# Optimization experiments

Measured on AMD Instinct MI355X. Metric: run time of the kernel, lower is better.

## Reference

```python
import jax, jax.numpy as jnp
import numpy as np

DIST_POWER = 1  # distance_power from init

def setup_inputs() -> dict:
    key = jax.random.key(0)
    k1, k2 = jax.random.split(key)
    N, D, C = 8192, 128, 256
    l_embeds = jax.random.normal(k1, (N, D), dtype=jnp.float32)
    l_labels = jax.random.randint(k2, (N,), 0, C, dtype=jnp.int64)
    return {"l_embeds": l_embeds, "l_labels": l_labels}

def reference(l_embeds, l_labels):
    # normalize_embeds=True
    x = l_embeds / jnp.linalg.norm(l_embeds, axis=1, keepdims=True)
    sq = jnp.sum(x * x, axis=1)  # [N]
    d2 = sq[:, None] + sq[None, :] - 2.0 * jnp.matmul(x, x.T)
    dist = jnp.sqrt(jnp.maximum(d2, 0.0))  # distance_power == 1
    if DIST_POWER != 1:
        dist = dist ** DIST_POWER
    N = x.shape[0]
    same = l_labels[:, None] == l_labels[None, :]
    eye = jnp.eye(N, dtype=bool)
    pos_mask = same & ~eye          # positives, diagonal removed (l is r)
    neg_mask = ~same
    # pos_dist = distmat * pos_mask (nan -> 0); hardest positive = argmax
    pos_dist = jnp.where(pos_mask, dist, 0.0)
    hardest_pos_inds = jnp.argmax(pos_dist, axis=1)
    # neg_dist = distmat with same-label entries set to +inf; hardest negative = argmin
    neg_dist = jnp.where(neg_mask, dist, jnp.inf)
    hardest_neg_inds = jnp.argmin(neg_dist, axis=1)
    anchor_inds = jnp.arange(N)
    # keep mask (all True by construction of labels); returned instead of
    # data-dependent boolean filtering to stay jit-compatible
    keep = jnp.any(pos_mask, axis=1) & jnp.any(neg_mask, axis=1)
    return anchor_inds, hardest_pos_inds, hardest_neg_inds, keep
```

## Files before the change

kernel.cpp:

```cpp
#include <hip/hip_runtime.h>
#include <math.h>

#define N 8192
#define D 128
#define C 256
#define CCAP 80
#define NT 64
#define NBLK (NT * (NT + 1) / 2)

typedef __attribute__((ext_vector_type(8))) short bf8;
typedef __attribute__((ext_vector_type(4))) float f4;

__device__ __forceinline__ unsigned short bf16_rtne(float f) {
    unsigned u = __float_as_uint(f);
    u += 0x7FFF + ((u >> 16) & 1);
    return (unsigned short)(u >> 16);
}
__device__ __forceinline__ float bf16_tof(unsigned short h) {
    return __uint_as_float((unsigned)h << 16);
}

__device__ __forceinline__ void async_cp16(const void* g, void* l) {
    __builtin_amdgcn_global_load_lds(
        (const __attribute__((address_space(1))) unsigned*)g,
        (__attribute__((address_space(3))) unsigned*)l, 16, 0, 0);
}

__device__ __forceinline__ unsigned int fbits(float f) {
    union { float f; unsigned int u; } x; x.f = f; return x.u;
}
__device__ __forceinline__ unsigned long long pack_pos(float v, int j) {
    return ((unsigned long long)fbits(v) << 32) | (unsigned int)(8191 - j);
}
__device__ __forceinline__ unsigned long long pack_neg(float v, int j) {
    return ((unsigned long long)fbits(v) << 32) | (unsigned int)j;
}
__device__ __forceinline__ void red_min(float& v, int& j, int mask) {
    const float ov = __shfl_xor(v, mask, 64);
    const int   oj = __shfl_xor(j, mask, 64);
    if (ov < v || (ov == v && oj < j)) { v = ov; j = oj; }
}

__global__ __launch_bounds__(256) void prep_kernel(
    const float* __restrict__ x, short* __restrict__ H,
    float* __restrict__ sq,
    unsigned long long* __restrict__ pos_pack,
    unsigned long long* __restrict__ neg_pack) {
    __shared__ float Xs[32 * 129];
    const int t = threadIdx.x;
    const int r0 = blockIdx.x * 32;

    if (t < 32) { pos_pack[r0 + t] = 0ULL; neg_pack[r0 + t] = ~0ULL; }

#pragma unroll
    for (int p = 0; p < 4; ++p) {
        const int lin = p * 256 + t;
        const int row = lin >> 5;
        const int c0 = (lin & 31) << 2;
        const float4 v = *(const float4*)(x + (size_t)(r0 + row) * D + c0);
        float* dst = &Xs[row * 129 + c0];
        dst[0] = v.x; dst[1] = v.y; dst[2] = v.z; dst[3] = v.w;
    }
    __syncthreads();

    const int r = t >> 3, q8 = t & 7;
    float* src = &Xs[r * 129 + q8 * 16];
    float s = 0.f;
#pragma unroll
    for (int i = 0; i < 16; ++i) s = fmaf(src[i], src[i], s);
    s += __shfl_xor(s, 1, 64);
    s += __shfl_xor(s, 2, 64);
    s += __shfl_xor(s, 4, 64);
    const float nrm = sqrtf(s);
    float t2 = 0.f;
#pragma unroll
    for (int i = 0; i < 16; ++i) {
        const float n = src[i] / nrm;
        src[i] = n;
        t2 = fmaf(n, n, t2);
    }
    t2 += __shfl_xor(t2, 1, 64);
    t2 += __shfl_xor(t2, 2, 64);
    t2 += __shfl_xor(t2, 4, 64);
    if (q8 == 0) sq[r0 + r] = t2;

    const size_t gbase = (size_t)(r0 + r) * D + q8 * 16;
#pragma unroll
    for (int g = 0; g < 4; ++g) {
        short4 o1, o2, o3;
        short* p1 = (short*)&o1; short* p2 = (short*)&o2; short* p3 = (short*)&o3;
#pragma unroll
        for (int i = 0; i < 4; ++i) {
            const float n = src[g * 4 + i];
            const unsigned short h1 = bf16_rtne(n);
            const float r1 = n - bf16_tof(h1);
            const unsigned short h2 = bf16_rtne(r1);
            const float r2 = r1 - bf16_tof(h2);
            const unsigned short h3 = bf16_rtne(r2);
            p1[i] = (short)h1; p2[i] = (short)h2; p3[i] = (short)h3;
        }
        *(short4*)(H + gbase + g * 4)                     = o1;
        *(short4*)(H + (size_t)N * D + gbase + g * 4)     = o2;
        *(short4*)(H + (size_t)2 * N * D + gbase + g * 4) = o3;
    }
}

union SMem {
    struct {
        short sB[2 * 12288];
        float sqS[256];
        int   lbS[256];
    } m;
    struct {
        float Xc[CCAP * 160];
        float Sq[CCAP];
        int   Rw[CCAP];
        int   n;
    } p;
};

__global__ __launch_bounds__(256, 3) void fused_kernel(
    const short* __restrict__ H, const float* __restrict__ sq,
    const int* __restrict__ labels,
    unsigned long long* __restrict__ pos_pack,
    unsigned long long* __restrict__ neg_pack) {
    __shared__ __align__(16) SMem sm;
    const int t = threadIdx.x;

    if (blockIdx.x < C) {
        const int c = blockIdx.x;
        const int k8 = t & 7;
        const int g  = t >> 3;

        if (t == 0) sm.p.n = 0;
        __syncthreads();
        for (int j = t; j < N; j += 256) {
            if (labels[j] == c) {
                const int s = atomicAdd(&sm.p.n, 1);
                if (s < CCAP) sm.p.Rw[s] = j;
            }
        }
        __syncthreads();
        const int n = min(sm.p.n, CCAP);

        for (int lin = t; lin < n * 16; lin += 256) {
            const int i = lin >> 4, cc = lin & 15;
            const short* h0 = H + (size_t)sm.p.Rw[i] * D + cc * 8;
            const bf8 L0 = *(const bf8*)h0;
            const bf8 L1 = *(const bf8*)(h0 + (size_t)N * D);
            const bf8 L2 = *(const bf8*)(h0 + (size_t)2 * N * D);
            float* dst = &sm.p.Xc[i * 160 + (cc >> 1) * 20 + (cc & 1) * 8];
#pragma unroll
            for (int j = 0; j < 8; ++j)
                dst[j] = bf16_tof((unsigned short)L0[j])
                       + bf16_tof((unsigned short)L1[j])
                       + bf16_tof((unsigned short)L2[j]);
        }
        if (t < n) sm.p.Sq[t] = sq[sm.p.Rw[t]];
        __syncthreads();

        for (int i = g; i < n; i += 32) {
            float xi[16];
#pragma unroll
            for (int d = 0; d < 16; ++d) xi[d] = sm.p.Xc[i * 160 + k8 * 20 + d];
            const float si = sm.p.Sq[i];
            float best = -1.0f; int bestj = 0x7FFFFFFF;
            for (int j = 0; j < n; ++j) {
                if (j == i) continue;
                const float* xj = &sm.p.Xc[j * 160 + k8 * 20];
                float p0 = 0.f, p1 = 0.f;
#pragma unroll
                for (int d = 0; d < 16; d += 2) {
                    p0 = fmaf(xi[d],     xj[d],     p0);
                    p1 = fmaf(xi[d + 1], xj[d + 1], p1);
                }
                float dot = p0 + p1;
                dot += __shfl_xor(dot, 1, 64);
                dot += __shfl_xor(dot, 2, 64);
                dot += __shfl_xor(dot, 4, 64);
                const float d2 = fmaxf(si + sm.p.Sq[j] - 2.0f * dot, 0.0f);
                const int rj = sm.p.Rw[j];
                if (d2 > best || (d2 == best && rj < bestj)) {
                    best = d2; bestj = rj;
                }
            }
            if (k8 == 0)
                pos_pack[sm.p.Rw[i]] = (best > 0.0f) ? pack_pos(best, bestj)
                                                     : pack_pos(0.0f, 0);
        }
        return;
    }

    const int w = t >> 6;
    const int l = t & 63;
    const int quad = l >> 4;
    const int l16 = l & 15;

    const int b0 = blockIdx.x - C;
    const int b  = (b0 & 7) * (NBLK / 8) + (b0 >> 3);
    int bi = (int)((129.0f - sqrtf(16641.0f - 8.0f * (float)b)) * 0.5f);
    while (bi > 0 && (bi * NT - bi * (bi - 1) / 2) > b) --bi;
    while (((bi + 1) * NT - (bi + 1) * bi / 2) <= b) ++bi;
    const int bj = bi + (b - (bi * NT - bi * (bi - 1) / 2));
    const int I0 = bi * 128, J0 = bj * 128;
    const bool diag = (bi == bj);

    float psq; int plb;
    {
        const int idx = ((t < 128) ? I0 : J0) + (t & 127);
        psq = sq[idx]; plb = labels[idx];
    }

    int gOffB[6], lOffB[6];
#pragma unroll
    for (int p = 0; p < 6; ++p) {
        const int limb = p >> 1;
        const int c2   = (p & 1) * 256 + t;
        const int smp  = c2 >> 2;
        const int sub  = c2 & 3;
        gOffB[p] = limb * (N * D) + (J0 + smp) * D + sub * 8;
        lOffB[p] = (limb * 128 + smp) * 32 + sub * 8;
    }
    int aGoff[3];
#pragma unroll
    for (int la = 0; la < 3; ++la)
        aGoff[la] = la * (N * D) + (I0 + w * 32 + l16) * D + quad * 8;

    f4 acc[2][8];
#pragma unroll
    for (int rt = 0; rt < 2; ++rt)
#pragma unroll
        for (int ct = 0; ct < 8; ++ct) acc[rt][ct] = (f4){0.f, 0.f, 0.f, 0.f};

    bf8 aF[2][3][2];
#pragma unroll
    for (int p = 0; p < 6; ++p)
        async_cp16(H + (size_t)gOffB[p], sm.m.sB + lOffB[p]);
#pragma unroll
    for (int la = 0; la < 3; ++la)
#pragma unroll
        for (int rt = 0; rt < 2; ++rt)
            aF[0][la][rt] = *(const bf8*)(H + (size_t)(aGoff[la] + rt * 2048));

#pragma unroll
    for (int q = 0; q < 4; ++q) {
        const int cur = q & 1, nxt = cur ^ 1;
        const short* sBc = sm.m.sB + cur * 12288;

        if (q < 3) {
            short* sBn = sm.m.sB + nxt * 12288;
            const int kn = (q + 1) * 32;
#pragma unroll
            for (int p = 0; p < 6; ++p)
                async_cp16(H + (size_t)(gOffB[p] + kn), sBn + lOffB[p]);
#pragma unroll
            for (int la = 0; la < 3; ++la)
#pragma unroll
                for (int rt = 0; rt < 2; ++rt)
                    aF[nxt][la][rt] = *(const bf8*)
                        (H + (size_t)(aGoff[la] + rt * 2048 + kn));
            asm volatile("s_waitcnt vmcnt(12)" ::: "memory");
        } else {
            asm volatile("s_waitcnt vmcnt(0)" ::: "memory");
        }
        __builtin_amdgcn_s_barrier();
        __builtin_amdgcn_sched_barrier(0);

        __builtin_amdgcn_s_setprio(1);
#pragma unroll
        for (int ct = 0; ct < 8; ++ct) {
            bf8 bF[3];
#pragma unroll
            for (int lb = 0; lb < 3; ++lb)
                bF[lb] = *(const bf8*)
                    &sBc[(lb * 128 + ct * 16 + l16) * 32 + quad * 8];
#pragma unroll
            for (int rt = 0; rt < 2; ++rt) {
                acc[rt][ct] = __builtin_amdgcn_mfma_f32_16x16x32_bf16(
                    aF[cur][0][rt], bF[0], acc[rt][ct], 0, 0, 0);
                acc[rt][ct] = __builtin_amdgcn_mfma_f32_16x16x32_bf16(
                    aF[cur][0][rt], bF[1], acc[rt][ct], 0, 0, 0);
                acc[rt][ct] = __builtin_amdgcn_mfma_f32_16x16x32_bf16(
                    aF[cur][0][rt], bF[2], acc[rt][ct], 0, 0, 0);
                acc[rt][ct] = __builtin_amdgcn_mfma_f32_16x16x32_bf16(
                    aF[cur][1][rt], bF[0], acc[rt][ct], 0, 0, 0);
                acc[rt][ct] = __builtin_amdgcn_mfma_f32_16x16x32_bf16(
                    aF[cur][1][rt], bF[1], acc[rt][ct], 0, 0, 0);
                acc[rt][ct] = __builtin_amdgcn_mfma_f32_16x16x32_bf16(
                    aF[cur][2][rt], bF[0], acc[rt][ct], 0, 0, 0);
            }
        }
        __builtin_amdgcn_s_setprio(0);

        if (q < 2) {
            asm volatile("" ::: "memory");
            __builtin_amdgcn_s_barrier();
            __builtin_amdgcn_sched_barrier(0);
        }
    }

    sm.m.sqS[t] = psq; sm.m.lbS[t] = plb;
    __syncthreads();
    const float* sqI = sm.m.sqS;  const float* sqJ = sm.m.sqS + 128;
    const int*   lbI = sm.m.lbS;  const int*   lbJ = sm.m.lbS + 128;

    int ljv[8];
#pragma unroll
    for (int ct = 0; ct < 8; ++ct) ljv[ct] = lbJ[ct * 16 + l16];

    {
        float sjv[8];
#pragma unroll
        for (int ct = 0; ct < 8; ++ct) sjv[ct] = sqJ[ct * 16 + l16];
#pragma unroll
        for (int rt = 0; rt < 2; ++rt)
#pragma unroll
            for (int r = 0; r < 4; ++r) {
                const float si = sqI[w * 32 + rt * 16 + quad * 4 + r];
#pragma unroll
                for (int ct = 0; ct < 8; ++ct)
                    acc[rt][ct][r] =
                        fmaxf(si + sjv[ct] - 2.0f * acc[rt][ct][r], 0.0f);
            }
    }

#pragma unroll
    for (int rt = 0; rt < 2; ++rt)
#pragma unroll
        for (int r = 0; r < 4; ++r) {
            const int lr = w * 32 + rt * 16 + quad * 4 + r;
            const int liv = lbI[lr];
            float bnv = INFINITY; int bnj = 0;
#pragma unroll
            for (int ct = 0; ct < 8; ++ct) {
                const float vn = (liv == ljv[ct]) ? INFINITY : acc[rt][ct][r];
                const int col = J0 + ct * 16 + l16;
                if (vn < bnv) { bnv = vn; bnj = col; }
            }
            red_min(bnv, bnj, 1); red_min(bnv, bnj, 2);
            red_min(bnv, bnj, 4); red_min(bnv, bnj, 8);
            if (l16 == 0)
                atomicMin(&neg_pack[I0 + lr], pack_neg(bnv, bnj));
        }

    if (!diag) {
        unsigned long long* scr = (unsigned long long*)sm.m.sB;
#pragma unroll
        for (int ct = 0; ct < 8; ++ct) {
            float bnv = INFINITY; int bnj = 0;
            const int lj = ljv[ct];
#pragma unroll
            for (int rt = 0; rt < 2; ++rt)
#pragma unroll
                for (int r = 0; r < 4; ++r) {
                    const int lr = w * 32 + rt * 16 + quad * 4 + r;
                    const float vn = (lbI[lr] == lj) ? INFINITY : acc[rt][ct][r];
                    if (vn < bnv) { bnv = vn; bnj = I0 + lr; }
                }
            red_min(bnv, bnj, 16); red_min(bnv, bnj, 32);
            if (quad == 0)
                scr[w * 128 + ct * 16 + l16] = pack_neg(bnv, bnj);
        }
        __syncthreads();
        if (t < 128) {
            unsigned long long mn = ~0ULL;
#pragma unroll
            for (int ww = 0; ww < 4; ++ww) {
                const unsigned long long qq = scr[ww * 128 + t];
                if (qq < mn) mn = qq;
            }
            atomicMin(&neg_pack[J0 + t], mn);
        }
    }
}

__global__ void finalize_kernel(const unsigned long long* __restrict__ pos_pack,
                                const unsigned long long* __restrict__ neg_pack,
                                int* __restrict__ out) {
    const int r = blockIdx.x * 256 + threadIdx.x;
    const unsigned long long pp = pos_pack[r];
    const unsigned long long np = neg_pack[r];
    out[r]         = r;
    out[N + r]     = 8191 - (int)(pp & 0xFFFFFFFFULL);
    out[2 * N + r] = (int)(np & 0xFFFFFFFFULL);
    out[3 * N + r] = (pp != 0ULL && np != ~0ULL) ? 1 : 0;
}

extern "C" void kernel_launch(void* const* d_in, const int* in_sizes, int n_in,
                              void* d_out, int out_size, void* d_ws, size_t ws_size,
                              hipStream_t stream) {
    const float* x      = (const float*)d_in[0];
    const int*   labels = (const int*)d_in[1];
    int* out = (int*)d_out;

    short* H = (short*)d_ws;
    float* sq = (float*)(H + (size_t)3 * N * D);
    unsigned long long* pos_pack =
        (unsigned long long*)(sq + N);
    unsigned long long* neg_pack = pos_pack + N;

    prep_kernel<<<N / 32, 256, 0, stream>>>(x, H, sq, pos_pack, neg_pack);
    fused_kernel<<<C + NBLK, 256, 0, stream>>>(H, sq, labels, pos_pack,
                                               neg_pack);
    finalize_kernel<<<N / 256, 256, 0, stream>>>(pos_pack, neg_pack, out);
}
```

Measured before the change: 136.8 us.

## Tile 128x128 block as 2x2 warp grid and prefetch A fragments after MFMA

Changes the per-wave output tile from 32 rows by 128 columns to 64 rows by 64 columns, so each wave reads only half the B tile from LDS and holds four A row-fragments. A-fragment double buffering is dropped: the next K-slice's A fragments are loaded from global memory into a single buffer after the MFMA block instead of before it, and the vmcnt wait is adjusted to match. The aim is to cut LDS read traffic per MFMA and free registers. The cost is less overlap of A global-load latency with compute, and the epilogue reductions and scratch layout must change to fit the new wave mapping.

```diff
diff --git a/kernel.cpp b/kernel.cpp
--- a/kernel.cpp
+++ b/kernel.cpp
@@ -195,6 +195,8 @@
     const int l = t & 63;
     const int quad = l >> 4;
     const int l16 = l & 15;
+    const int rowHalf = w & 1;
+    const int colHalf = w >> 1;
 
     const int b0 = blockIdx.x - C;
     const int b  = (b0 & 7) * (NBLK / 8) + (b0 >> 3);
@@ -224,23 +226,23 @@
     int aGoff[3];
 #pragma unroll
     for (int la = 0; la < 3; ++la)
-        aGoff[la] = la * (N * D) + (I0 + w * 32 + l16) * D + quad * 8;
-
-    f4 acc[2][8];
-#pragma unroll
-    for (int rt = 0; rt < 2; ++rt)
-#pragma unroll
-        for (int ct = 0; ct < 8; ++ct) acc[rt][ct] = (f4){0.f, 0.f, 0.f, 0.f};
-
-    bf8 aF[2][3][2];
+        aGoff[la] = la * (N * D) + (I0 + rowHalf * 64 + l16) * D + quad * 8;
+
+    f4 acc[4][4];
+#pragma unroll
+    for (int rt = 0; rt < 4; ++rt)
+#pragma unroll
+        for (int ct = 0; ct < 4; ++ct) acc[rt][ct] = (f4){0.f, 0.f, 0.f, 0.f};
+
+    bf8 aF[3][4];
 #pragma unroll
     for (int p = 0; p < 6; ++p)
         async_cp16(H + (size_t)gOffB[p], sm.m.sB + lOffB[p]);
 #pragma unroll
     for (int la = 0; la < 3; ++la)
 #pragma unroll
-        for (int rt = 0; rt < 2; ++rt)
-            aF[0][la][rt] = *(const bf8*)(H + (size_t)(aGoff[la] + rt * 2048));
+        for (int rt = 0; rt < 4; ++rt)
+            aF[la][rt] = *(const bf8*)(H + (size_t)(aGoff[la] + rt * 2048));
 
 #pragma unroll
     for (int q = 0; q < 4; ++q) {
@@ -253,13 +255,7 @@
 #pragma unroll
             for (int p = 0; p < 6; ++p)
                 async_cp16(H + (size_t)(gOffB[p] + kn), sBn + lOffB[p]);
-#pragma unroll
-            for (int la = 0; la < 3; ++la)
-#pragma unroll
-                for (int rt = 0; rt < 2; ++rt)
-                    aF[nxt][la][rt] = *(const bf8*)
-                        (H + (size_t)(aGoff[la] + rt * 2048 + kn));
-            asm volatile("s_waitcnt vmcnt(12)" ::: "memory");
+            asm volatile("s_waitcnt vmcnt(18)" ::: "memory");
         } else {
             asm volatile("s_waitcnt vmcnt(0)" ::: "memory");
         }
@@ -268,29 +264,40 @@
 
         __builtin_amdgcn_s_setprio(1);
 #pragma unroll
-        for (int ct = 0; ct < 8; ++ct) {
+        for (int ct = 0; ct < 4; ++ct) {
             bf8 bF[3];
 #pragma unroll
             for (int lb = 0; lb < 3; ++lb)
                 bF[lb] = *(const bf8*)
-                    &sBc[(lb * 128 + ct * 16 + l16) * 32 + quad * 8];
-#pragma unroll
-            for (int rt = 0; rt < 2; ++rt) {
-                acc[rt][ct] = __builtin_amdgcn_mfma_f32_16x16x32_bf16(
-                    aF[cur][0][rt], bF[0], acc[rt][ct], 0, 0, 0);
-                acc[rt][ct] = __builtin_amdgcn_mfma_f32_16x16x32_bf16(
-                    aF[cur][0][rt], bF[1], acc[rt][ct], 0, 0, 0);
-                acc[rt][ct] = __builtin_amdgcn_mfma_f32_16x16x32_bf16(
-                    aF[cur][0][rt], bF[2], acc[rt][ct], 0, 0, 0);
-                acc[rt][ct] = __builtin_amdgcn_mfma_f32_16x16x32_bf16(
-                    aF[cur][1][rt], bF[0], acc[rt][ct], 0, 0, 0);
-                acc[rt][ct] = __builtin_amdgcn_mfma_f32_16x16x32_bf16(
-                    aF[cur][1][rt], bF[1], acc[rt][ct], 0, 0, 0);
-                acc[rt][ct] = __builtin_amdgcn_mfma_f32_16x16x32_bf16(
-                    aF[cur][2][rt], bF[0], acc[rt][ct], 0, 0, 0);
+                    &sBc[(lb * 128 + colHalf * 64 + ct * 16 + l16) * 32
+                         + quad * 8];
+#pragma unroll
+            for (int rt = 0; rt < 4; ++rt) {
+                acc[rt][ct] = __builtin_amdgcn_mfma_f32_16x16x32_bf16(
+                    aF[0][rt], bF[0], acc[rt][ct], 0, 0, 0);
+                acc[rt][ct] = __builtin_amdgcn_mfma_f32_16x16x32_bf16(
+                    aF[0][rt], bF[1], acc[rt][ct], 0, 0, 0);
+                acc[rt][ct] = __builtin_amdgcn_mfma_f32_16x16x32_bf16(
+                    aF[0][rt], bF[2], acc[rt][ct], 0, 0, 0);
+                acc[rt][ct] = __builtin_amdgcn_mfma_f32_16x16x32_bf16(
+                    aF[1][rt], bF[0], acc[rt][ct], 0, 0, 0);
+                acc[rt][ct] = __builtin_amdgcn_mfma_f32_16x16x32_bf16(
+                    aF[1][rt], bF[1], acc[rt][ct], 0, 0, 0);
+                acc[rt][ct] = __builtin_amdgcn_mfma_f32_16x16x32_bf16(
+                    aF[2][rt], bF[0], acc[rt][ct], 0, 0, 0);
             }
         }
         __builtin_amdgcn_s_setprio(0);
+
+        if (q < 3) {
+            const int kn2 = (q + 1) * 32;
+#pragma unroll
+            for (int la = 0; la < 3; ++la)
+#pragma unroll
+                for (int rt = 0; rt < 4; ++rt)
+                    aF[la][rt] = *(const bf8*)
+                        (H + (size_t)(aGoff[la] + rt * 2048 + kn2));
+        }
 
         if (q < 2) {
             asm volatile("" ::: "memory");
@@ -304,37 +311,39 @@
     const float* sqI = sm.m.sqS;  const float* sqJ = sm.m.sqS + 128;
     const int*   lbI = sm.m.lbS;  const int*   lbJ = sm.m.lbS + 128;
 
-    int ljv[8];
-#pragma unroll
-    for (int ct = 0; ct < 8; ++ct) ljv[ct] = lbJ[ct * 16 + l16];
+    int ljv[4];
+#pragma unroll
+    for (int ct = 0; ct < 4; ++ct)
+        ljv[ct] = lbJ[colHalf * 64 + ct * 16 + l16];
 
     {
-        float sjv[8];
-#pragma unroll
-        for (int ct = 0; ct < 8; ++ct) sjv[ct] = sqJ[ct * 16 + l16];
-#pragma unroll
-        for (int rt = 0; rt < 2; ++rt)
+        float sjv[4];
+#pragma unroll
+        for (int ct = 0; ct < 4; ++ct)
+            sjv[ct] = sqJ[colHalf * 64 + ct * 16 + l16];
+#pragma unroll
+        for (int rt = 0; rt < 4; ++rt)
 #pragma unroll
             for (int r = 0; r < 4; ++r) {
-                const float si = sqI[w * 32 + rt * 16 + quad * 4 + r];
-#pragma unroll
-                for (int ct = 0; ct < 8; ++ct)
+                const float si = sqI[rowHalf * 64 + rt * 16 + quad * 4 + r];
+#pragma unroll
+                for (int ct = 0; ct < 4; ++ct)
                     acc[rt][ct][r] =
                         fmaxf(si + sjv[ct] - 2.0f * acc[rt][ct][r], 0.0f);
             }
     }
 
 #pragma unroll
-    for (int rt = 0; rt < 2; ++rt)
+    for (int rt = 0; rt < 4; ++rt)
 #pragma unroll
         for (int r = 0; r < 4; ++r) {
-            const int lr = w * 32 + rt * 16 + quad * 4 + r;
+            const int lr = rowHalf * 64 + rt * 16 + quad * 4 + r;
             const int liv = lbI[lr];
             float bnv = INFINITY; int bnj = 0;
 #pragma unroll
-            for (int ct = 0; ct < 8; ++ct) {
+            for (int ct = 0; ct < 4; ++ct) {
                 const float vn = (liv == ljv[ct]) ? INFINITY : acc[rt][ct][r];
-                const int col = J0 + ct * 16 + l16;
+                const int col = J0 + colHalf * 64 + ct * 16 + l16;
                 if (vn < bnv) { bnv = vn; bnj = col; }
             }
             red_min(bnv, bnj, 1); red_min(bnv, bnj, 2);
@@ -346,30 +355,27 @@
     if (!diag) {
         unsigned long long* scr = (unsigned long long*)sm.m.sB;
 #pragma unroll
-        for (int ct = 0; ct < 8; ++ct) {
+        for (int ct = 0; ct < 4; ++ct) {
             float bnv = INFINITY; int bnj = 0;
             const int lj = ljv[ct];
 #pragma unroll
-            for (int rt = 0; rt < 2; ++rt)
+            for (int rt = 0; rt < 4; ++rt)
 #pragma unroll
                 for (int r = 0; r < 4; ++r) {
-                    const int lr = w * 32 + rt * 16 + quad * 4 + r;
+                    const int lr = rowHalf * 64 + rt * 16 + quad * 4 + r;
                     const float vn = (lbI[lr] == lj) ? INFINITY : acc[rt][ct][r];
                     if (vn < bnv) { bnv = vn; bnj = I0 + lr; }
                 }
             red_min(bnv, bnj, 16); red_min(bnv, bnj, 32);
             if (quad == 0)
-                scr[w * 128 + ct * 16 + l16] = pack_neg(bnv, bnj);
+                scr[w * 64 + ct * 16 + l16] = pack_neg(bnv, bnj);
         }
         __syncthreads();
         if (t < 128) {
-            unsigned long long mn = ~0ULL;
-#pragma unroll
-            for (int ww = 0; ww < 4; ++ww) {
-                const unsigned long long qq = scr[ww * 128 + t];
-                if (qq < mn) mn = qq;
-            }
-            atomicMin(&neg_pack[J0 + t], mn);
+            const int half = t >> 6, lc = t & 63;
+            const unsigned long long m1 = scr[(2 * half) * 64 + lc];
+            const unsigned long long m2 = scr[(2 * half + 1) * 64 + lc];
+            atomicMin(&neg_pack[J0 + t], m1 < m2 ? m1 : m2);
         }
     }
 }
```

After: 167.9 us. 22.7% more time.
